# Kernel optimization log

Measured on AMD Instinct MI355X. Metric: run time of the kernel, lower is better.

Reference implementation:

```python
import jax, jax.numpy as jnp
import numpy as np

B, L, SD, PD, H, HD, OH = 2, 256, 64, 32, 4, 16, 32
EXP = 64  # MBConv hidden = pair_dim * expand_ratio(2)
SE = 16   # squeezed channels = int(64 * 0.25)


def _ln(x, g, b, eps=1e-5):
    m = jnp.mean(x, -1, keepdims=True)
    v = jnp.mean((x - m) ** 2, -1, keepdims=True)
    return (x - m) / jnp.sqrt(v + eps) * g + b


def _inorm(x, eps=1e-5):  # InstanceNorm2d (no affine), x: [B,C,H,W]
    m = jnp.mean(x, (2, 3), keepdims=True)
    v = jnp.mean((x - m) ** 2, (2, 3), keepdims=True)
    return (x - m) / jnp.sqrt(v + eps)


def setup_inputs() -> dict:
    key = jax.random.key(0)
    ks = jax.random.split(key, 16)
    s = jnp.float32(0.02)
    return dict(
        seq_repr=jax.random.normal(ks[0], (B, L, SD), jnp.float32),
        pair_repr=jax.random.normal(ks[1], (B, L, L, PD), jnp.float32),
        g_attn=jnp.ones((SD,), jnp.float32), b_attn=jnp.zeros((SD,), jnp.float32),
        g_pair=jnp.ones((PD,), jnp.float32), b_pair=jnp.zeros((PD,), jnp.float32),
        W_opm_lin=jax.random.normal(ks[2], (SD, OH), jnp.float32) * s,
        b_opm_lin=jnp.zeros((OH,), jnp.float32),
        g_opm=jnp.ones((OH * OH,), jnp.float32), b_opm=jnp.zeros((OH * OH,), jnp.float32),
        W_opm_proj=jax.random.normal(ks[3], (OH * OH, PD), jnp.float32) * s,
        b_opm_proj=jnp.zeros((PD,), jnp.float32),
        W_exp=jax.random.normal(ks[4], (EXP, PD), jnp.float32) * s,
        W_dw=jax.random.normal(ks[5], (EXP, 1, 3, 3), jnp.float32) * s,
        W_se1=jax.random.normal(ks[6], (SE, EXP), jnp.float32) * s,
        b_se1=jnp.zeros((SE,), jnp.float32),
        W_se2=jax.random.normal(ks[7], (EXP, SE), jnp.float32) * s,
        b_se2=jnp.zeros((EXP,), jnp.float32),
        W_pw=jax.random.normal(ks[8], (PD, EXP), jnp.float32) * s,
        W_qkv=jax.random.normal(ks[9], (SD, 3 * SD), jnp.float32) * s,
        W_outp=jax.random.normal(ks[10], (SD, SD), jnp.float32) * s,
        b_outp=jnp.zeros((SD,), jnp.float32),
        W_bias=jax.random.normal(ks[11], (PD, H), jnp.float32) * s,
    )


def reference(seq_repr, pair_repr, g_attn, b_attn, g_pair, b_pair,
              W_opm_lin, b_opm_lin, g_opm, b_opm, W_opm_proj, b_opm_proj,
              W_exp, W_dw, W_se1, b_se1, W_se2, b_se2, W_pw,
              W_qkv, W_outp, b_outp, W_bias):
    # --- OuterProductMean on attn_norm(seq) ---
    x = _ln(seq_repr, g_attn, b_attn)                            # [B,L,SD]
    a = x @ W_opm_lin + b_opm_lin                                # [B,L,OH]
    outer = jnp.einsum('bid,bje->bijde', a, a).reshape(B, L, L, OH * OH)
    op = _ln(outer, g_opm, b_opm) @ W_opm_proj + b_opm_proj      # [B,L,L,PD]
    pair = pair_repr + op
    # --- MBConv pair processor on pair_norm(pair) ---
    pn = _ln(pair, g_pair, b_pair)
    z0 = jnp.transpose(pn, (0, 3, 1, 2))                         # NCHW [B,PD,L,L]
    h = jax.nn.silu(_inorm(jnp.einsum('bcij,oc->boij', z0, W_exp)))
    h = jax.lax.conv_general_dilated(h, W_dw, (1, 1), 'SAME',
                                     feature_group_count=EXP,
                                     dimension_numbers=('NCHW', 'OIHW', 'NCHW'))
    h = jax.nn.silu(_inorm(h))
    sq = jnp.mean(h, (2, 3), keepdims=True)                      # squeeze [B,EXP,1,1]
    sq = jax.nn.silu(jnp.einsum('bcij,oc->boij', sq, W_se1) + b_se1[None, :, None, None])
    sq = jax.nn.sigmoid(jnp.einsum('bcij,oc->boij', sq, W_se2) + b_se2[None, :, None, None])
    h = h * sq
    h = _inorm(jnp.einsum('bcij,oc->boij', h, W_pw))             # project back to PD
    pair = pair + jnp.transpose(z0 + h, (0, 2, 3, 1))            # MBConv residual + outer residual
    # --- Pairwise-bias attention ---
    pn2 = _ln(pair, g_pair, b_pair)
    bias = jnp.einsum('bijp,ph->bhij', pn2, W_bias)              # [B,H,L,L]
    q, k, v = jnp.split(x @ W_qkv, 3, axis=-1)
    q = q.reshape(B, L, H, HD).transpose(0, 2, 1, 3)
    k = k.reshape(B, L, H, HD).transpose(0, 2, 1, 3)
    v = v.reshape(B, L, H, HD).transpose(0, 2, 1, 3)
    scores = jnp.einsum('bhid,bhjd->bhij', q, k) / jnp.sqrt(jnp.float32(HD)) + bias
    w = jax.nn.softmax(scores, axis=-1)
    ctx = jnp.einsum('bhij,bhjd->bhid', w, v).transpose(0, 2, 1, 3).reshape(B, L, SD)
    seq = seq_repr + ctx @ W_outp + b_outp
    return seq, pair
```

## Files before the change

kernel.cpp:

```cpp
#include <hip/hip_runtime.h>
#include <hip/hip_bf16.h>

#define LLSZ 65536
#define INV_LL (1.f / 65536.f)


__device__ __forceinline__ void chan_stats(const float* sum, const float* sumsq,
                                           int chan, float& m, float& isd)
{
    m = sum[chan] * INV_LL;
    float var = sumsq[chan] * INV_LL - m * m;
    isd = rsqrtf(var + 1e-5f);
}

__device__ __forceinline__ float silu(float t) { return t / (1.f + expf(-t)); }

__global__ __launch_bounds__(256) void kA(
    const float* __restrict__ g_opm, const float* __restrict__ b_opm,
    const float* __restrict__ Wproj, const float* __restrict__ b_proj,
    float* __restrict__ G, float* __restrict__ GW, float* __restrict__ BW,
    float* __restrict__ stats0,
    const float* __restrict__ seq, const float* __restrict__ g_attn,
    const float* __restrict__ b_attn, const float* __restrict__ W_lin,
    const float* __restrict__ b_lin, const float* __restrict__ W_qkv,
    float* __restrict__ a, float* __restrict__ am, float* __restrict__ s2,
    float* __restrict__ qkv)
{
    int tid = threadIdx.x;
    if (blockIdx.x == 0) {
        for (int k = tid; k < 768; k += 256) stats0[k] = 0.f;
        int p = tid & 31, rg = tid >> 5;
        float gw = 0.f, bw = 0.f;
        #pragma unroll 8
        for (int k = 0; k < 128; ++k) {
            int de = k * 8 + rg;
            float wv = Wproj[de * 32 + p];
            float gv = g_opm[de] * wv;
            G[de * 32 + p] = gv;
            gw += gv;
            bw += b_opm[de] * wv;
        }
        __shared__ float rG[256], rB[256];
        rG[rg * 32 + p] = gw;
        rB[rg * 32 + p] = bw;
        __syncthreads();
        for (int s = 4; s > 0; s >>= 1) {
            if (rg < s) {
                rG[rg * 32 + p] += rG[(rg + s) * 32 + p];
                rB[rg * 32 + p] += rB[(rg + s) * 32 + p];
            }
            __syncthreads();
        }
        if (tid < 32) { GW[p] = rG[p]; BW[p] = rB[p] + b_proj[p]; }
    } else {
        __shared__ float Wq[64 * 192];
        __shared__ float Wl[64 * 32];
        __shared__ float xL[4][64];
        #pragma unroll
        for (int k = 0; k < 48; ++k) Wq[k * 256 + tid] = W_qkv[k * 256 + tid];
        #pragma unroll
        for (int k = 0; k < 8; ++k) Wl[k * 256 + tid] = W_lin[k * 256 + tid];
        int sub = tid >> 6, t = tid & 63;
        int row = (blockIdx.x - 1) * 4 + sub;
        float v = seq[row * 64 + t];
        float m = v;
        for (int k = 32; k > 0; k >>= 1) m += __shfl_xor(m, k, 64);
        m *= (1.f / 64.f);
        float d = v - m;
        float var = d * d;
        for (int k = 32; k > 0; k >>= 1) var += __shfl_xor(var, k, 64);
        var *= (1.f / 64.f);
        float x = d * rsqrtf(var + 1e-5f) * g_attn[t] + b_attn[t];
        xL[sub][t] = x;
        __syncthreads();
        if (t < 32) {
            float s = 0.f;
            #pragma unroll
            for (int dd = 0; dd < 64; ++dd) s += xL[sub][dd] * Wl[dd * 32 + t];
            s += b_lin[t];
            a[row * 32 + t] = s;
            float mm = s, ss = s * s;
            for (int k = 16; k > 0; k >>= 1) {
                mm += __shfl_xor(mm, k, 32);
                ss += __shfl_xor(ss, k, 32);
            }
            if (t == 0) { am[row] = mm * (1.f / 32.f); s2[row] = ss * (1.f / 32.f); }
        }
        #pragma unroll
        for (int c3 = 0; c3 < 3; ++c3) {
            int c = c3 * 64 + t;
            float s = 0.f;
            #pragma unroll
            for (int dd = 0; dd < 64; ++dd) s += xL[sub][dd] * Wq[dd * 192 + c];
            qkv[row * 192 + c] = s;
        }
    }
}

__global__ __launch_bounds__(256) void k2_T(
    const float* __restrict__ a, const float* __restrict__ G, float* __restrict__ T)
{
    int row = blockIdx.x;
    int tid = threadIdx.x;
    __shared__ float aL[32];
    if (tid < 32) aL[tid] = a[row * 32 + tid];
    __syncthreads();
    for (int k = 0; k < 4; ++k) {
        int idx = k * 256 + tid;
        float s = 0.f;
        #pragma unroll
        for (int d = 0; d < 32; ++d) s += aL[d] * G[d * 1024 + idx];
        T[row * 1024 + idx] = s;
    }
}

__global__ __launch_bounds__(256) void k3_op(
    const float* __restrict__ a, const float* __restrict__ am,
    const float* __restrict__ s2, const float* __restrict__ T,
    const float* __restrict__ GW, const float* __restrict__ BW,
    const float* __restrict__ pair_in, float* __restrict__ pair1)
{
    int blk = blockIdx.x;
    int row = blk >> 3;
    int jg = blk & 7;
    int b = row >> 8;
    int j0 = jg * 32;
    int tid = threadIdx.x;
    __shared__ float Tl[1024];
    __shared__ float aL[32 * 33];
    __shared__ float amL[32], s2L[32], gwL[32], bwL[32];
    ((float4*)Tl)[tid] = ((const float4*)(T + (long)row * 1024))[tid];
    for (int k = 0; k < 4; ++k) {
        int idx = k * 256 + tid;
        aL[(idx >> 5) * 33 + (idx & 31)] = a[(b * 256 + j0) * 32 + idx];
    }
    if (tid < 32) {
        amL[tid] = am[b * 256 + j0 + tid];
        s2L[tid] = s2[b * 256 + j0 + tid];
        gwL[tid] = GW[tid];
        bwL[tid] = BW[tid];
    }
    __syncthreads();
    int jl = tid >> 3, cq = tid & 7;
    float am_i = am[row], s2_i = s2[row];
    float m = am_i * amL[jl];
    float isd = rsqrtf(s2_i * s2L[jl] - m * m + 1e-5f);
    long base = ((long)row * 256 + j0 + jl) * 32 + cq * 4;
    float4 pv = *(const float4*)(pair_in + base);
    float o[4];
    #pragma unroll
    for (int u = 0; u < 4; ++u) {
        int p = cq * 4 + u;
        float S = 0.f;
        #pragma unroll
        for (int e = 0; e < 32; ++e) S += aL[jl * 33 + e] * Tl[e * 32 + p];
        o[u] = isd * (S - m * gwL[p]) + bwL[p];
    }
    pv.x += o[0]; pv.y += o[1]; pv.z += o[2]; pv.w += o[3];
    *(float4*)(pair1 + base) = pv;
}

__global__ __launch_bounds__(256) void k4_expand(
    const float* __restrict__ pair1, const float* __restrict__ g_pair,
    const float* __restrict__ b_pair, const float* __restrict__ W_exp,
    float* __restrict__ e1)
{
    int b = blockIdx.x >> 10;
    int px0 = (blockIdx.x & 1023) * 64;
    int tid = threadIdx.x;
    __shared__ float pnL[64 * 33];
    #pragma unroll
    for (int k = 0; k < 2; ++k) {
        int idx = k * 256 + tid;
        int px = idx >> 3, cq = idx & 7;
        float4 v = *(const float4*)(pair1 + ((long)b * LLSZ + px0 + px) * 32 + cq * 4);
        pnL[px * 33 + cq * 4 + 0] = v.x;
        pnL[px * 33 + cq * 4 + 1] = v.y;
        pnL[px * 33 + cq * 4 + 2] = v.z;
        pnL[px * 33 + cq * 4 + 3] = v.w;
    }
    __syncthreads();
    int px = tid & 63, og = tid >> 6;
    float x[32];
    #pragma unroll
    for (int c = 0; c < 32; ++c) x[c] = pnL[px * 33 + c];
    float s = 0.f, q = 0.f;
    #pragma unroll
    for (int c = 0; c < 32; ++c) { s += x[c]; q += x[c] * x[c]; }
    float mu = s * (1.f / 32.f);
    float isd = rsqrtf(q * (1.f / 32.f) - mu * mu + 1e-5f);
    #pragma unroll
    for (int c = 0; c < 32; ++c)
        x[c] = (x[c] - mu) * isd * g_pair[c] + b_pair[c];
    float* dst = e1 + ((long)(b * 64 + og * 16)) * LLSZ + px0 + px;
    #pragma unroll
    for (int k = 0; k < 16; ++k) {
        int o = og * 16 + k;
        float acc = 0.f;
        #pragma unroll
        for (int c = 0; c < 32; ++c) acc += x[c] * W_exp[o * 32 + c];
        dst[(long)k * LLSZ] = acc;
    }
}

__global__ __launch_bounds__(256) void k_stats(
    const float* __restrict__ buf, float* __restrict__ sum, float* __restrict__ sumsq)
{
    int bid = blockIdx.x;
    int chan = bid >> 3, seg = bid & 7;
    int tid = threadIdx.x;
    const float4* p = (const float4*)(buf + (long)chan * LLSZ + seg * 8192);
    float s = 0.f, ss = 0.f;
    #pragma unroll
    for (int k = 0; k < 8; ++k) {
        float4 v = p[k * 256 + tid];
        s += v.x + v.y + v.z + v.w;
        ss += v.x * v.x + v.y * v.y + v.z * v.z + v.w * v.w;
    }
    for (int k = 32; k > 0; k >>= 1) { s += __shfl_xor(s, k, 64); ss += __shfl_xor(ss, k, 64); }
    __shared__ float rs[4], rq[4];
    int wave = tid >> 6;
    if ((tid & 63) == 0) { rs[wave] = s; rq[wave] = ss; }
    __syncthreads();
    if (tid == 0) {
        atomicAdd(&sum[chan], rs[0] + rs[1] + rs[2] + rs[3]);
        atomicAdd(&sumsq[chan], rq[0] + rq[1] + rq[2] + rq[3]);
    }
}

__global__ __launch_bounds__(256) void k6_dw(
    const float* __restrict__ e1, const float* __restrict__ st1s,
    const float* __restrict__ st1q, const float* __restrict__ W_dw,
    float* __restrict__ h2, float* __restrict__ st2s, float* __restrict__ st2q)
{
    int blk = blockIdx.x;
    int chan = blk >> 5;
    int r0 = (blk & 31) * 8;
    int o = chan & 63;
    int tid = threadIdx.x;
    float m, isd;
    chan_stats(st1s, st1q, chan, m, isd);
    __shared__ float sL[10][258];
    const float* src = e1 + (long)chan * LLSZ;
    for (int k = tid; k < 640; k += 256) {
        int rr = k >> 6, c4 = k & 63;
        int g = r0 - 1 + rr;
        float4 v = make_float4(0.f, 0.f, 0.f, 0.f);
        bool ok = (g >= 0 && g < 256);
        if (ok) v = *(const float4*)(src + g * 256 + c4 * 4);
        float t;
        t = (v.x - m) * isd; v.x = ok ? silu(t) : 0.f;
        t = (v.y - m) * isd; v.y = ok ? silu(t) : 0.f;
        t = (v.z - m) * isd; v.z = ok ? silu(t) : 0.f;
        t = (v.w - m) * isd; v.w = ok ? silu(t) : 0.f;
        sL[rr][1 + c4 * 4 + 0] = v.x;
        sL[rr][1 + c4 * 4 + 1] = v.y;
        sL[rr][1 + c4 * 4 + 2] = v.z;
        sL[rr][1 + c4 * 4 + 3] = v.w;
    }
    if (tid < 10) { sL[tid][0] = 0.f; sL[tid][257] = 0.f; }
    float w[9];
    #pragma unroll
    for (int k = 0; k < 9; ++k) w[k] = W_dw[o * 9 + k];
    __syncthreads();
    int c = tid;
    float bs = 0.f, bq = 0.f;
    #pragma unroll
    for (int rr = 0; rr < 8; ++rr) {
        float s = 0.f;
        #pragma unroll
        for (int ki = 0; ki < 3; ++ki)
            #pragma unroll
            for (int kj = 0; kj < 3; ++kj)
                s += sL[rr + ki][c + kj] * w[ki * 3 + kj];
        h2[(long)chan * LLSZ + (r0 + rr) * 256 + c] = s;
        bs += s; bq += s * s;
    }
    for (int k = 32; k > 0; k >>= 1) { bs += __shfl_xor(bs, k, 64); bq += __shfl_xor(bq, k, 64); }
    __shared__ float r2s[4], r2q[4];
    int wave = tid >> 6;
    if ((tid & 63) == 0) { r2s[wave] = bs; r2q[wave] = bq; }
    __syncthreads();
    if (tid == 0) {
        atomicAdd(&st2s[chan], r2s[0] + r2s[1] + r2s[2] + r2s[3]);
        atomicAdd(&st2q[chan], r2q[0] + r2q[1] + r2q[2] + r2q[3]);
    }
}

__global__ __launch_bounds__(256) void k8_squeeze(
    const float* __restrict__ h2, const float* __restrict__ st2s,
    const float* __restrict__ st2q, float* __restrict__ sqs)
{
    int bid = blockIdx.x;
    int chan = bid >> 3, seg = bid & 7;
    int tid = threadIdx.x;
    float m, isd;
    chan_stats(st2s, st2q, chan, m, isd);
    const float4* p = (const float4*)(h2 + (long)chan * LLSZ + seg * 8192);
    float s = 0.f;
    #pragma unroll
    for (int k = 0; k < 8; ++k) {
        float4 v = p[k * 256 + tid];
        s += silu((v.x - m) * isd) + silu((v.y - m) * isd)
           + silu((v.z - m) * isd) + silu((v.w - m) * isd);
    }
    for (int k = 32; k > 0; k >>= 1) s += __shfl_xor(s, k, 64);
    __shared__ float rs[4];
    int wave = tid >> 6;
    if ((tid & 63) == 0) rs[wave] = s;
    __syncthreads();
    if (tid == 0) atomicAdd(&sqs[chan], rs[0] + rs[1] + rs[2] + rs[3]);
}

__global__ __launch_bounds__(256) void k10_pw(
    const float* __restrict__ h2, const float* __restrict__ st2s,
    const float* __restrict__ st2q, const float* __restrict__ sqs,
    const float* __restrict__ W_se1, const float* __restrict__ b_se1,
    const float* __restrict__ W_se2, const float* __restrict__ b_se2,
    const float* __restrict__ W_pw, float* __restrict__ hp)
{
    int b = blockIdx.x >> 10;
    int px0 = (blockIdx.x & 1023) * 64;
    int tid = threadIdx.x;
    __shared__ float s1L[16];
    __shared__ float sqvL[64], mL[64], iL[64];
    __shared__ float hL[64 * 64];
    if (tid < 16) {
        float s = 0.f;
        for (int c = 0; c < 64; ++c) s += sqs[b * 64 + c] * W_se1[tid * 64 + c];
        s = s * INV_LL + b_se1[tid];
        s1L[tid] = silu(s);
    }
    __syncthreads();
    if (tid < 64) {
        float s = 0.f;
        #pragma unroll
        for (int j = 0; j < 16; ++j) s += s1L[j] * W_se2[tid * 16 + j];
        s += b_se2[tid];
        sqvL[tid] = 1.f / (1.f + expf(-s));
        float m, isd;
        chan_stats(st2s, st2q, b * 64 + tid, m, isd);
        mL[tid] = m; iL[tid] = isd;
    }
    __syncthreads();
    #pragma unroll
    for (int k = 0; k < 4; ++k) {
        int idx = k * 256 + tid;
        int c = idx >> 4, cq = idx & 15;
        float m = mL[c], isd = iL[c], sc = sqvL[c];
        float4 v = *(const float4*)(h2 + (long)(b * 64 + c) * LLSZ + px0 + cq * 4);
        v.x = silu((v.x - m) * isd) * sc;
        v.y = silu((v.y - m) * isd) * sc;
        v.z = silu((v.z - m) * isd) * sc;
        v.w = silu((v.w - m) * isd) * sc;
        *(float4*)(hL + c * 64 + cq * 4) = v;
    }
    __syncthreads();
    int px = tid & 63, og = tid >> 6;
    float acc[8];
    #pragma unroll
    for (int u = 0; u < 8; ++u) acc[u] = 0.f;
    #pragma unroll
    for (int c = 0; c < 64; ++c) {
        float x = hL[c * 64 + px];
        #pragma unroll
        for (int u = 0; u < 8; ++u) acc[u] += x * W_pw[(og * 8 + u) * 64 + c];
    }
    float* dst = hp + ((long)(b * 32 + og * 8)) * LLSZ + px0 + px;
    #pragma unroll
    for (int u = 0; u < 8; ++u) dst[(long)u * LLSZ] = acc[u];
}

__global__ __launch_bounds__(256) void k12_merge(
    const float* __restrict__ pair1, const float* __restrict__ hp,
    const float* __restrict__ st3s, const float* __restrict__ st3q,
    const float* __restrict__ g_pair, const float* __restrict__ b_pair,
    const float* __restrict__ W_bias, float* __restrict__ pair_out,
    float* __restrict__ biasbuf)
{
    int b = blockIdx.x >> 10;
    int px0 = (blockIdx.x & 1023) * 64;
    int tid = threadIdx.x;
    __shared__ float pnL[64 * 33];
    __shared__ float hpN[32 * 65];
    #pragma unroll
    for (int k = 0; k < 2; ++k) {
        int idx = k * 256 + tid;
        int px = idx >> 3, cq = idx & 7;
        float4 v = *(const float4*)(pair1 + ((long)b * LLSZ + px0 + px) * 32 + cq * 4);
        pnL[px * 33 + cq * 4 + 0] = v.x;
        pnL[px * 33 + cq * 4 + 1] = v.y;
        pnL[px * 33 + cq * 4 + 2] = v.z;
        pnL[px * 33 + cq * 4 + 3] = v.w;
    }
    #pragma unroll
    for (int k = 0; k < 2; ++k) {
        int idx = k * 256 + tid;
        int c = idx >> 4, cq = idx & 15;
        float m3, isd3;
        chan_stats(st3s, st3q, b * 32 + c, m3, isd3);
        float4 v = *(const float4*)(hp + (long)(b * 32 + c) * LLSZ + px0 + cq * 4);
        hpN[c * 65 + cq * 4 + 0] = (v.x - m3) * isd3;
        hpN[c * 65 + cq * 4 + 1] = (v.y - m3) * isd3;
        hpN[c * 65 + cq * 4 + 2] = (v.z - m3) * isd3;
        hpN[c * 65 + cq * 4 + 3] = (v.w - m3) * isd3;
    }
    __syncthreads();
    int px = tid >> 2, part = tid & 3;
    float v1[8];
    #pragma unroll
    for (int u = 0; u < 8; ++u) v1[u] = pnL[px * 33 + part * 8 + u];
    float s = 0.f, q = 0.f;
    #pragma unroll
    for (int u = 0; u < 8; ++u) { s += v1[u]; q += v1[u] * v1[u]; }
    s += __shfl_xor(s, 1, 4); q += __shfl_xor(q, 1, 4);
    s += __shfl_xor(s, 2, 4); q += __shfl_xor(q, 2, 4);
    float mu = s * (1.f / 32.f);
    float isd = rsqrtf(q * (1.f / 32.f) - mu * mu + 1e-5f);
    float vo[8];
    #pragma unroll
    for (int u = 0; u < 8; ++u) {
        int c = part * 8 + u;
        float pnv = (v1[u] - mu) * isd * g_pair[c] + b_pair[c];
        vo[u] = v1[u] + pnv + hpN[c * 65 + px];
    }
    long obase = ((long)b * LLSZ + px0 + px) * 32 + part * 8;
    *(float4*)(pair_out + obase)     = make_float4(vo[0], vo[1], vo[2], vo[3]);
    *(float4*)(pair_out + obase + 4) = make_float4(vo[4], vo[5], vo[6], vo[7]);
    float s2_ = 0.f, q2 = 0.f;
    #pragma unroll
    for (int u = 0; u < 8; ++u) { s2_ += vo[u]; q2 += vo[u] * vo[u]; }
    s2_ += __shfl_xor(s2_, 1, 4); q2 += __shfl_xor(q2, 1, 4);
    s2_ += __shfl_xor(s2_, 2, 4); q2 += __shfl_xor(q2, 2, 4);
    float mu2 = s2_ * (1.f / 32.f);
    float isd2 = rsqrtf(q2 * (1.f / 32.f) - mu2 * mu2 + 1e-5f);
    float t[4] = {0.f, 0.f, 0.f, 0.f};
    #pragma unroll
    for (int u = 0; u < 8; ++u) {
        int c = part * 8 + u;
        float pn2 = (vo[u] - mu2) * isd2 * g_pair[c] + b_pair[c];
        #pragma unroll
        for (int h = 0; h < 4; ++h) t[h] += pn2 * W_bias[c * 4 + h];
    }
    #pragma unroll
    for (int h = 0; h < 4; ++h) {
        t[h] += __shfl_xor(t[h], 1, 4);
        t[h] += __shfl_xor(t[h], 2, 4);
    }
    if (part == 0) {
        #pragma unroll
        for (int h = 0; h < 4; ++h)
            biasbuf[((long)(b * 4 + h)) * LLSZ + px0 + px] = t[h];
    }
}

__global__ __launch_bounds__(256) void k13_attn(
    const float* __restrict__ qkv, const float* __restrict__ biasbuf,
    float* __restrict__ ctx)
{
    int blk = blockIdx.x;
    int b = blk >> 8;
    int h = (blk >> 6) & 3;
    int ig = blk & 63;
    int tid = threadIdx.x;
    int wave = tid >> 6, lane = tid & 63;
    __shared__ float kL[16][256];
    __shared__ float vL[16][256];
    {
        const float4* kr = (const float4*)(qkv + ((long)(b * 256 + tid)) * 192 + 64 + h * 16);
        float4 k0 = kr[0], k1 = kr[1], k2 = kr[2], k3 = kr[3];
        const float4* vr = (const float4*)(qkv + ((long)(b * 256 + tid)) * 192 + 128 + h * 16);
        float4 w0 = vr[0], w1 = vr[1], w2 = vr[2], w3 = vr[3];
        kL[ 0][tid] = k0.x; kL[ 1][tid] = k0.y; kL[ 2][tid] = k0.z; kL[ 3][tid] = k0.w;
        kL[ 4][tid] = k1.x; kL[ 5][tid] = k1.y; kL[ 6][tid] = k1.z; kL[ 7][tid] = k1.w;
        kL[ 8][tid] = k2.x; kL[ 9][tid] = k2.y; kL[10][tid] = k2.z; kL[11][tid] = k2.w;
        kL[12][tid] = k3.x; kL[13][tid] = k3.y; kL[14][tid] = k3.z; kL[15][tid] = k3.w;
        vL[ 0][tid] = w0.x; vL[ 1][tid] = w0.y; vL[ 2][tid] = w0.z; vL[ 3][tid] = w0.w;
        vL[ 4][tid] = w1.x; vL[ 5][tid] = w1.y; vL[ 6][tid] = w1.z; vL[ 7][tid] = w1.w;
        vL[ 8][tid] = w2.x; vL[ 9][tid] = w2.y; vL[10][tid] = w2.z; vL[11][tid] = w2.w;
        vL[12][tid] = w3.x; vL[13][tid] = w3.y; vL[14][tid] = w3.z; vL[15][tid] = w3.w;
    }
    __syncthreads();
    int i = ig * 4 + wave;
    const float* qrow = qkv + ((long)(b * 256 + i)) * 192 + h * 16;
    float qv[16];
    #pragma unroll
    for (int d = 0; d < 16; ++d) qv[d] = qrow[d];
    float sj[4];
    #pragma unroll
    for (int q = 0; q < 4; ++q) {
        int j = 64 * q + lane;
        float s = 0.f;
        #pragma unroll
        for (int d = 0; d < 16; ++d) s += qv[d] * kL[d][j];
        sj[q] = s * 0.25f + biasbuf[((long)(b * 4 + h)) * LLSZ + i * 256 + j];
    }
    float mx = fmaxf(fmaxf(sj[0], sj[1]), fmaxf(sj[2], sj[3]));
    for (int k = 32; k > 0; k >>= 1) mx = fmaxf(mx, __shfl_xor(mx, k, 64));
    float wgt[4], wsum = 0.f;
    #pragma unroll
    for (int q = 0; q < 4; ++q) { wgt[q] = expf(sj[q] - mx); wsum += wgt[q]; }
    for (int k = 32; k > 0; k >>= 1) wsum += __shfl_xor(wsum, k, 64);
    float inv = 1.f / wsum;
    float o[16];
    #pragma unroll
    for (int d = 0; d < 16; ++d) o[d] = 0.f;
    #pragma unroll
    for (int q = 0; q < 4; ++q) {
        int j = 64 * q + lane;
        #pragma unroll
        for (int d = 0; d < 16; ++d) o[d] += wgt[q] * vL[d][j];
    }
    #pragma unroll
    for (int d = 0; d < 16; ++d)
        for (int k = 32; k > 0; k >>= 1) o[d] += __shfl_xor(o[d], k, 64);
    if (lane == 0) {
        #pragma unroll
        for (int d = 0; d < 16; ++d)
            ctx[((long)(b * 256 + i)) * 64 + h * 16 + d] = o[d] * inv;
    }
}

__global__ __launch_bounds__(256) void k14_seqout(
    const float* __restrict__ seq, const float* __restrict__ ctx,
    const float* __restrict__ W_outp, const float* __restrict__ b_outp,
    float* __restrict__ out)
{
    __shared__ float Wo[64 * 64];
    __shared__ float cL[4][64];
    int tid = threadIdx.x;
    #pragma unroll
    for (int k = 0; k < 16; ++k) Wo[k * 256 + tid] = W_outp[k * 256 + tid];
    int sub = tid >> 6, t = tid & 63;
    int row = blockIdx.x * 4 + sub;
    cL[sub][t] = ctx[row * 64 + t];
    __syncthreads();
    float s = b_outp[t];
    #pragma unroll
    for (int u = 0; u < 64; ++u) s += cL[sub][u] * Wo[u * 64 + t];
    out[row * 64 + t] = seq[row * 64 + t] + s;
}

extern "C" void kernel_launch(void* const* d_in, const int* in_sizes, int n_in,
                              void* d_out, int out_size, void* d_ws, size_t ws_size,
                              hipStream_t stream) {
    const float* seq_repr   = (const float*)d_in[0];
    const float* pair_repr  = (const float*)d_in[1];
    const float* g_attn     = (const float*)d_in[2];
    const float* b_attn     = (const float*)d_in[3];
    const float* g_pair     = (const float*)d_in[4];
    const float* b_pair     = (const float*)d_in[5];
    const float* W_opm_lin  = (const float*)d_in[6];
    const float* b_opm_lin  = (const float*)d_in[7];
    const float* g_opm      = (const float*)d_in[8];
    const float* b_opm      = (const float*)d_in[9];
    const float* W_opm_proj = (const float*)d_in[10];
    const float* b_opm_proj = (const float*)d_in[11];
    const float* W_exp      = (const float*)d_in[12];
    const float* W_dw       = (const float*)d_in[13];
    const float* W_se1      = (const float*)d_in[14];
    const float* b_se1      = (const float*)d_in[15];
    const float* W_se2      = (const float*)d_in[16];
    const float* b_se2      = (const float*)d_in[17];
    const float* W_pw       = (const float*)d_in[18];
    const float* W_qkv      = (const float*)d_in[19];
    const float* W_outp     = (const float*)d_in[20];
    const float* b_outp     = (const float*)d_in[21];
    const float* W_bias     = (const float*)d_in[22];

    float* out_seq  = (float*)d_out;
    float* out_pair = (float*)d_out + 32768;

    float* w = (float*)d_ws;
    float* a_buf   = w;
    float* am_buf  = a_buf + 16384;
    float* s2_buf  = am_buf + 512;
    float* qkv_buf = s2_buf + 512;
    float* G_buf   = qkv_buf + 98304;
    float* GW_buf  = G_buf + 32768;
    float* BW_buf  = GW_buf + 32;
    float* ctx     = BW_buf + 32;
    float* st1s    = ctx + 32768;
    float* st1q    = st1s + 128;
    float* st2s    = st1q + 128;
    float* st2q    = st2s + 128;
    float* st3s    = st2q + 128;
    float* st3q    = st3s + 64;
    float* sqs     = st3q + 64;
    float* T_buf   = sqs + 128;
    float* biasb   = T_buf;
    float* pair1   = T_buf + 524288;
    float* e1      = pair1 + 4194304;
    float* hp      = e1;
    float* h2      = e1 + 8388608;

    hipLaunchKernelGGL(kA, dim3(129), dim3(256), 0, stream,
                       g_opm, b_opm, W_opm_proj, b_opm_proj, G_buf, GW_buf, BW_buf,
                       st1s,
                       seq_repr, g_attn, b_attn, W_opm_lin, b_opm_lin, W_qkv,
                       a_buf, am_buf, s2_buf, qkv_buf);
    hipLaunchKernelGGL(k2_T, dim3(512), dim3(256), 0, stream, a_buf, G_buf, T_buf);
    hipLaunchKernelGGL(k3_op, dim3(4096), dim3(256), 0, stream,
                       a_buf, am_buf, s2_buf, T_buf, GW_buf, BW_buf,
                       pair_repr, pair1);
    hipLaunchKernelGGL(k4_expand, dim3(2048), dim3(256), 0, stream,
                       pair1, g_pair, b_pair, W_exp, e1);
    hipLaunchKernelGGL(k_stats, dim3(1024), dim3(256), 0, stream, e1, st1s, st1q);
    hipLaunchKernelGGL(k6_dw, dim3(4096), dim3(256), 0, stream,
                       e1, st1s, st1q, W_dw, h2, st2s, st2q);
    hipLaunchKernelGGL(k8_squeeze, dim3(1024), dim3(256), 0, stream,
                       h2, st2s, st2q, sqs);
    hipLaunchKernelGGL(k10_pw, dim3(2048), dim3(256), 0, stream,
                       h2, st2s, st2q, sqs, W_se1, b_se1, W_se2, b_se2,
                       W_pw, hp);
    hipLaunchKernelGGL(k_stats, dim3(512), dim3(256), 0, stream, hp, st3s, st3q);
    hipLaunchKernelGGL(k12_merge, dim3(2048), dim3(256), 0, stream,
                       pair1, hp, st3s, st3q, g_pair, b_pair, W_bias,
                       out_pair, biasb);
    hipLaunchKernelGGL(k13_attn, dim3(512), dim3(256), 0, stream,
                       qkv_buf, biasb, ctx);
    hipLaunchKernelGGL(k14_seqout, dim3(128), dim3(256), 0, stream,
                       seq_repr, ctx, W_outp, b_outp, out_seq);
}
```

Before: 299.2 us.

## Fuse instance-norm channel statistics into expand and pointwise kernels

Removes the two standalone k_stats passes. The expand and pointwise-projection kernels now reduce per-channel sum and sum-of-squares with wave shuffles right after computing their outputs, then atomically add them into the stats buffers. This avoids re-reading the large e1 and hp tensors from memory and saves two launches. The cost is extra shuffle reductions and more atomics (one per channel per wave rather than per block), which could contend. It also marks og as wave-uniform with readfirstlane so weight loads can become scalar.

Result: slower. 325.9 us (+8.9%).

```diff
diff --git a/kernel.cpp b/kernel.cpp
--- a/kernel.cpp
+++ b/kernel.cpp
@@ -163,7 +163,7 @@
 __global__ __launch_bounds__(256) void k4_expand(
     const float* __restrict__ pair1, const float* __restrict__ g_pair,
     const float* __restrict__ b_pair, const float* __restrict__ W_exp,
-    float* __restrict__ e1)
+    float* __restrict__ e1, float* __restrict__ st1s, float* __restrict__ st1q)
 {
     int b = blockIdx.x >> 10;
     int px0 = (blockIdx.x & 1023) * 64;
@@ -180,7 +180,8 @@
         pnL[px * 33 + cq * 4 + 3] = v.w;
     }
     __syncthreads();
-    int px = tid & 63, og = tid >> 6;
+    int px = tid & 63;
+    int og = __builtin_amdgcn_readfirstlane(tid >> 6);
     float x[32];
     #pragma unroll
     for (int c = 0; c < 32; ++c) x[c] = pnL[px * 33 + c];
@@ -193,6 +194,7 @@
     for (int c = 0; c < 32; ++c)
         x[c] = (x[c] - mu) * isd * g_pair[c] + b_pair[c];
     float* dst = e1 + ((long)(b * 64 + og * 16)) * LLSZ + px0 + px;
+    float ssk = 0.f, qqk = 0.f;
     #pragma unroll
     for (int k = 0; k < 16; ++k) {
         int o = og * 16 + k;
@@ -200,31 +202,16 @@
         #pragma unroll
         for (int c = 0; c < 32; ++c) acc += x[c] * W_exp[o * 32 + c];
         dst[(long)k * LLSZ] = acc;
-    }
-}
-
-__global__ __launch_bounds__(256) void k_stats(
-    const float* __restrict__ buf, float* __restrict__ sum, float* __restrict__ sumsq)
-{
-    int bid = blockIdx.x;
-    int chan = bid >> 3, seg = bid & 7;
-    int tid = threadIdx.x;
-    const float4* p = (const float4*)(buf + (long)chan * LLSZ + seg * 8192);
-    float s = 0.f, ss = 0.f;
-    #pragma unroll
-    for (int k = 0; k < 8; ++k) {
-        float4 v = p[k * 256 + tid];
-        s += v.x + v.y + v.z + v.w;
-        ss += v.x * v.x + v.y * v.y + v.z * v.z + v.w * v.w;
-    }
-    for (int k = 32; k > 0; k >>= 1) { s += __shfl_xor(s, k, 64); ss += __shfl_xor(ss, k, 64); }
-    __shared__ float rs[4], rq[4];
-    int wave = tid >> 6;
-    if ((tid & 63) == 0) { rs[wave] = s; rq[wave] = ss; }
-    __syncthreads();
-    if (tid == 0) {
-        atomicAdd(&sum[chan], rs[0] + rs[1] + rs[2] + rs[3]);
-        atomicAdd(&sumsq[chan], rq[0] + rq[1] + rq[2] + rq[3]);
+        float rs = acc, rq = acc * acc;
+        for (int sft = 32; sft > 0; sft >>= 1) {
+            rs += __shfl_xor(rs, sft, 64);
+            rq += __shfl_xor(rq, sft, 64);
+        }
+        if (px == k) { ssk = rs; qqk = rq; }
+    }
+    if (px < 16) {
+        atomicAdd(&st1s[b * 64 + og * 16 + px], ssk);
+        atomicAdd(&st1q[b * 64 + og * 16 + px], qqk);
     }
 }
 
@@ -317,7 +304,8 @@
     const float* __restrict__ st2q, const float* __restrict__ sqs,
     const float* __restrict__ W_se1, const float* __restrict__ b_se1,
     const float* __restrict__ W_se2, const float* __restrict__ b_se2,
-    const float* __restrict__ W_pw, float* __restrict__ hp)
+    const float* __restrict__ W_pw, float* __restrict__ hp,
+    float* __restrict__ st3s, float* __restrict__ st3q)
 {
     int b = blockIdx.x >> 10;
     int px0 = (blockIdx.x & 1023) * 64;
@@ -356,7 +344,8 @@
         *(float4*)(hL + c * 64 + cq * 4) = v;
     }
     __syncthreads();
-    int px = tid & 63, og = tid >> 6;
+    int px = tid & 63;
+    int og = __builtin_amdgcn_readfirstlane(tid >> 6);
     float acc[8];
     #pragma unroll
     for (int u = 0; u < 8; ++u) acc[u] = 0.f;
@@ -367,8 +356,21 @@
         for (int u = 0; u < 8; ++u) acc[u] += x * W_pw[(og * 8 + u) * 64 + c];
     }
     float* dst = hp + ((long)(b * 32 + og * 8)) * LLSZ + px0 + px;
-    #pragma unroll
-    for (int u = 0; u < 8; ++u) dst[(long)u * LLSZ] = acc[u];
+    float ssk = 0.f, qqk = 0.f;
+    #pragma unroll
+    for (int u = 0; u < 8; ++u) {
+        dst[(long)u * LLSZ] = acc[u];
+        float rs = acc[u], rq = acc[u] * acc[u];
+        for (int sft = 32; sft > 0; sft >>= 1) {
+            rs += __shfl_xor(rs, sft, 64);
+            rq += __shfl_xor(rq, sft, 64);
+        }
+        if (px == u) { ssk = rs; qqk = rq; }
+    }
+    if (px < 8) {
+        atomicAdd(&st3s[b * 32 + og * 8 + px], ssk);
+        atomicAdd(&st3q[b * 32 + og * 8 + px], qqk);
+    }
 }
 
 __global__ __launch_bounds__(256) void k12_merge(
@@ -604,16 +606,14 @@
                        a_buf, am_buf, s2_buf, T_buf, GW_buf, BW_buf,
                        pair_repr, pair1);
     hipLaunchKernelGGL(k4_expand, dim3(2048), dim3(256), 0, stream,
-                       pair1, g_pair, b_pair, W_exp, e1);
-    hipLaunchKernelGGL(k_stats, dim3(1024), dim3(256), 0, stream, e1, st1s, st1q);
+                       pair1, g_pair, b_pair, W_exp, e1, st1s, st1q);
     hipLaunchKernelGGL(k6_dw, dim3(4096), dim3(256), 0, stream,
                        e1, st1s, st1q, W_dw, h2, st2s, st2q);
     hipLaunchKernelGGL(k8_squeeze, dim3(1024), dim3(256), 0, stream,
                        h2, st2s, st2q, sqs);
     hipLaunchKernelGGL(k10_pw, dim3(2048), dim3(256), 0, stream,
                        h2, st2s, st2q, sqs, W_se1, b_se1, W_se2, b_se2,
-                       W_pw, hp);
-    hipLaunchKernelGGL(k_stats, dim3(512), dim3(256), 0, stream, hp, st3s, st3q);
+                       W_pw, hp, st3s, st3q);
     hipLaunchKernelGGL(k12_merge, dim3(2048), dim3(256), 0, stream,
                        pair1, hp, st3s, st3q, g_pair, b_pair, W_bias,
                        out_pair, biasb);
```
